# Performance work log

Measured on AMD Instinct MI355X. Metric: run time of the kernel, lower is better.

## Reference

```python
import jax, jax.numpy as jnp
import numpy as np

B, S, H = 2, 4096, 2048
NH, HD = 16, 128
BLOCK = 256
EPS = 1e-5


def setup_inputs() -> dict:
    key = jax.random.key(0)
    ks = jax.random.split(key, 6)
    return {
        "hidden_states": jax.random.normal(ks[0], (B, S, H), jnp.float32),
        "attention_mask": jnp.ones((B, S), jnp.float32),
        "slope_rate": jax.random.uniform(ks[1], (NH,), jnp.float32),
        "w_qkv": jax.random.normal(ks[2], (H, 3 * NH * HD), jnp.float32) * 0.02,
        "w_gate": jax.random.normal(ks[3], (H, NH * HD), jnp.float32) * 0.02,
        "w_out": jax.random.normal(ks[4], (NH * HD, H), jnp.float32) * 0.02,
        "norm_weight": jnp.ones((NH * HD,), jnp.float32),
    }


def _lightning_attention(q, k, v, slope):
    # q,k,v: [b,h,n,d]; slope: [h] positive decay rates
    b, h, n, d = q.shape
    nc = n // BLOCK
    ar = jnp.arange(BLOCK, dtype=q.dtype) + 1.0  # 1..BLOCK
    s = slope[:, None, None]  # [h,1,1]
    q_decay = jnp.exp(-s * ar[None, :, None])             # [h,BLOCK,1]
    k_decay = jnp.exp(-s * (BLOCK - ar)[None, :, None])   # [h,BLOCK,1]
    idx = ar[:, None] - ar[None, :]                        # [BLOCK,BLOCK]
    mask = (idx >= 0).astype(q.dtype)
    # mask idx before exp so masked entries don't overflow (keeps grads finite)
    diag_decay = jnp.exp(-s * (idx * mask)[None]) * mask[None]  # [h,BLOCK,BLOCK]
    block_decay = jnp.exp(-slope * BLOCK)[None, :, None, None]  # [1,h,1,1]

    def to_chunks(x):
        return x.reshape(b, h, nc, BLOCK, d).transpose(2, 0, 1, 3, 4)

    qc, kc, vc = to_chunks(q), to_chunks(k), to_chunks(v)

    def step(kv, xs):
        qi, ki, vi = xs  # [b,h,BLOCK,d]
        # inter-chunk: decayed query against carried state kv [b,h,d,d]
        o_inter = jnp.einsum("bhmd,bhde->bhme", qi * q_decay, kv)
        # intra-chunk: causal decayed attention
        attn = jnp.einsum("bhmd,bhnd->bhmn", qi, ki) * diag_decay
        o = o_inter + jnp.einsum("bhmn,bhne->bhme", attn, vi)
        kv = block_decay * kv + jnp.einsum("bhnd,bhne->bhde", ki * k_decay, vi)
        return kv, o

    kv0 = jnp.zeros((b, h, d, d), q.dtype)
    _, o = jax.lax.scan(step, kv0, (qc, kc, vc))  # o: [nc,b,h,BLOCK,d]
    return o.transpose(1, 2, 0, 3, 4).reshape(b, h, n, d)


def reference(hidden_states, attention_mask, slope_rate, w_qkv, w_gate, w_out, norm_weight):
    b, n, _ = hidden_states.shape
    qkv = jax.nn.silu(hidden_states @ w_qkv)  # act on fused qkv
    q, k, v = jnp.split(qkv, 3, axis=-1)

    def heads(x):
        return x.reshape(b, n, NH, HD).transpose(0, 2, 1, 3)

    q, k, v = heads(q), heads(k), heads(v)
    v = v * attention_mask[:, None, :, None]  # zero padded tokens
    o = _lightning_attention(q, k, v, slope_rate)  # [b,h,n,d]
    o = o.transpose(0, 2, 1, 3).reshape(b, n, NH * HD)
    # RMSNorm over head_dim*num_heads
    var = jnp.mean(o * o, axis=-1, keepdims=True)
    o = o * jax.lax.rsqrt(var + EPS) * norm_weight
    # sigmoid output gate from raw hidden_states
    o = jax.nn.sigmoid(hidden_states @ w_gate) * o
    return o @ w_out
```

## Files before the change

kernel.cpp:

```cpp
#include <hip/hip_runtime.h>
#include <cstdint>

#define B_ 2
#define S_ 4096
#define H_ 2048
#define NH_ 16
#define HD_ 128
#define BLOCK_ 256
#define NC_ (S_/BLOCK_)
#define M_ (B_*S_)
#define EPS_ 1e-5f

typedef unsigned short ushort_t;
typedef unsigned short u16x4 __attribute__((ext_vector_type(4)));
typedef short frag_ab __attribute__((ext_vector_type(8)));
typedef float frag_cd __attribute__((ext_vector_type(4)));

static __device__ inline float bf2f(ushort_t u) {
    union { unsigned int i; float f; } x;
    x.i = ((unsigned int)u) << 16;
    return x.f;
}
static __device__ inline ushort_t f2bf(float f) {
    union { float f; unsigned int i; } x;
    x.f = f;
    unsigned int r = x.i + 0x7fffu + ((x.i >> 16) & 1u);
    return (ushort_t)(r >> 16);
}

static __device__ __forceinline__ void gload_lds16(const ushort_t* g, ushort_t* l) {
    __builtin_amdgcn_global_load_lds(
        (__attribute__((address_space(1))) void*)(uintptr_t)g,
        (__attribute__((address_space(3))) void*)l,
        16, 0, 0);
}

#define FENCE_ asm volatile("" ::: "memory")
#define VMW0_  asm volatile("s_waitcnt vmcnt(0)" ::: "memory")

__global__ __launch_bounds__(256)
void cast_bf16_kernel(const float* __restrict__ in, ushort_t* __restrict__ out)
{
    int i = blockIdx.x * 256 + threadIdx.x;
    float4 v = reinterpret_cast<const float4*>(in)[i];
    u16x4 o = { f2bf(v.x), f2bf(v.y), f2bf(v.z), f2bf(v.w) };
    *reinterpret_cast<u16x4*>(&out[(size_t)i * 4]) = o;
}

__global__ __launch_bounds__(256)
void transpose_cast_kernel(const float* __restrict__ W, ushort_t* __restrict__ WT,
                           int K, int N)
{
    __shared__ float t[32][33];
    const int kb = blockIdx.y * 32, nb = blockIdx.x * 32;
    const int tx = threadIdx.x & 31, ty = threadIdx.x >> 5;
    #pragma unroll
    for (int i = 0; i < 4; ++i)
        t[ty + i * 8][tx] = W[(size_t)(kb + ty + i * 8) * N + nb + tx];
    __syncthreads();
    #pragma unroll
    for (int i = 0; i < 4; ++i)
        WT[(size_t)(nb + ty + i * 8) * K + kb + tx] = f2bf(t[tx][ty + i * 8]);
}

template<int MODE>
__global__ __launch_bounds__(512, 2)
void gemm256(const ushort_t* __restrict__ A, const ushort_t* __restrict__ BT,
             int M, int N, int K,
             float* __restrict__ Cf,
             ushort_t* __restrict__ qo, ushort_t* __restrict__ ko,
             ushort_t* __restrict__ kTo, ushort_t* __restrict__ vTo,
             ushort_t* __restrict__ gateo, const float* __restrict__ mask)
{
    __shared__ __align__(16) ushort_t LA[2][16384];
    __shared__ __align__(16) ushort_t LB[2][16384];

    const int tid  = threadIdx.x;
    const int lane = tid & 63, wid = tid >> 6;
    const int wm = wid >> 2, wn = wid & 3;
    const int l15 = lane & 15, l4 = lane >> 4;
    const int trow = tid >> 3;
    const int xk   = (tid & 7) ^ (trow & 7);

    const int lin = blockIdx.x;
    const int NBX = N >> 8;
    const int bxw = NBX >> 3;
    const int xcd = lin & 7, cc = lin >> 3;
    const int sh  = (bxw == 4) ? 2 : 0;
    const int by  = cc >> sh;
    const int bxi = cc & (bxw - 1);
    const int bx  = xcd * bxw + bxi;
    const int rowBase = by * 256, colBase = bx * 256;

    frag_cd acc[8][4];
    #pragma unroll
    for (int m = 0; m < 8; ++m)
        #pragma unroll
        for (int n = 0; n < 4; ++n) acc[m][n] = 0.f;

    frag_ab fa[4][2];
    frag_ab fb[2][2][2];

    #define RDF(Lp, row_, sl_) \
        (*reinterpret_cast<const frag_ab*>( \
            reinterpret_cast<const char*>(Lp) + (row_) * 128 + ((((sl_) ^ ((row_) & 7)) & 7) << 4)))
    #define STG(Gp, base_, i_, kt_, Lp) \
        gload_lds16((Gp) + (size_t)((base_) + (i_) * 64 + trow) * K + (kt_) + xk * 8, \
                    (Lp) + (i_) * 4096 + wid * 512)

    const int NT = K >> 6;
    int cur = 0;
    STG(BT, colBase, 0, 0, LB[0]); STG(BT, colBase, 1, 0, LB[0]);
    STG(BT, colBase, 2, 0, LB[0]); STG(BT, colBase, 3, 0, LB[0]);
    STG(A,  rowBase, 0, 0, LA[0]); STG(A,  rowBase, 1, 0, LA[0]);
    STG(A,  rowBase, 2, 0, LA[0]); STG(A,  rowBase, 3, 0, LA[0]);
    VMW0_; FENCE_; __builtin_amdgcn_s_barrier();
    __builtin_amdgcn_sched_barrier(0);

    for (int t = 0; t < NT; ++t) {
        const ushort_t* Ab = LA[cur];
        const ushort_t* Bb = LB[cur];
        ushort_t* An = LA[cur ^ 1];
        ushort_t* Bn = LB[cur ^ 1];
        const int ktn = (t + 1) << 6;
        const bool more = (t + 1) < NT;

        if (more) {
            STG(BT, colBase, 0, ktn, Bn); STG(BT, colBase, 1, ktn, Bn);
            STG(BT, colBase, 2, ktn, Bn); STG(BT, colBase, 3, ktn, Bn);
            STG(A,  rowBase, 0, ktn, An); STG(A,  rowBase, 1, ktn, An);
            STG(A,  rowBase, 2, ktn, An); STG(A,  rowBase, 3, ktn, An);
        }

        #pragma unroll
        for (int mi = 0; mi < 4; ++mi)
            #pragma unroll
            for (int ks = 0; ks < 2; ++ks)
                fa[mi][ks] = RDF(Ab, wm * 128 + mi * 16 + l15, ks * 4 + l4);
        #pragma unroll
        for (int ni = 0; ni < 2; ++ni)
            #pragma unroll
            for (int ks = 0; ks < 2; ++ks)
                fb[0][ni][ks] = RDF(Bb, wn * 64 + ni * 16 + l15, ks * 4 + l4);
        __builtin_amdgcn_s_setprio(1);
        #pragma unroll
        for (int mi = 0; mi < 4; ++mi)
            #pragma unroll
            for (int ni = 0; ni < 2; ++ni)
                #pragma unroll
                for (int ks = 0; ks < 2; ++ks)
                    acc[mi][ni] = __builtin_amdgcn_mfma_f32_16x16x32_bf16(
                        fa[mi][ks], fb[0][ni][ks], acc[mi][ni], 0, 0, 0);
        __builtin_amdgcn_s_setprio(0);

        #pragma unroll
        for (int ni = 0; ni < 2; ++ni)
            #pragma unroll
            for (int ks = 0; ks < 2; ++ks)
                fb[1][ni][ks] = RDF(Bb, wn * 64 + 32 + ni * 16 + l15, ks * 4 + l4);
        __builtin_amdgcn_s_setprio(1);
        #pragma unroll
        for (int mi = 0; mi < 4; ++mi)
            #pragma unroll
            for (int ni = 0; ni < 2; ++ni)
                #pragma unroll
                for (int ks = 0; ks < 2; ++ks)
                    acc[mi][2 + ni] = __builtin_amdgcn_mfma_f32_16x16x32_bf16(
                        fa[mi][ks], fb[1][ni][ks], acc[mi][2 + ni], 0, 0, 0);
        __builtin_amdgcn_s_setprio(0);

        #pragma unroll
        for (int mi = 0; mi < 4; ++mi)
            #pragma unroll
            for (int ks = 0; ks < 2; ++ks)
                fa[mi][ks] = RDF(Ab, wm * 128 + 64 + mi * 16 + l15, ks * 4 + l4);
        __builtin_amdgcn_s_setprio(1);
        #pragma unroll
        for (int mi = 0; mi < 4; ++mi)
            #pragma unroll
            for (int ni = 0; ni < 2; ++ni)
                #pragma unroll
                for (int ks = 0; ks < 2; ++ks)
                    acc[4 + mi][ni] = __builtin_amdgcn_mfma_f32_16x16x32_bf16(
                        fa[mi][ks], fb[0][ni][ks], acc[4 + mi][ni], 0, 0, 0);
        __builtin_amdgcn_s_setprio(0);

        __builtin_amdgcn_s_setprio(1);
        #pragma unroll
        for (int mi = 0; mi < 4; ++mi)
            #pragma unroll
            for (int ni = 0; ni < 2; ++ni)
                #pragma unroll
                for (int ks = 0; ks < 2; ++ks)
                    acc[4 + mi][2 + ni] = __builtin_amdgcn_mfma_f32_16x16x32_bf16(
                        fa[mi][ks], fb[1][ni][ks], acc[4 + mi][2 + ni], 0, 0, 0);
        __builtin_amdgcn_s_setprio(0);

        VMW0_; FENCE_; __builtin_amdgcn_s_barrier();
        __builtin_amdgcn_sched_barrier(0);
        cur ^= 1;
    }
    #undef RDF
    #undef STG

    const int row0 = rowBase + wm * 128;
    const int c0   = colBase + wn * 64;
    if (MODE == 0) {
        #pragma unroll
        for (int m = 0; m < 8; ++m) {
            int mr = (m >> 2) * 64 + (m & 3) * 16;
            #pragma unroll
            for (int n = 0; n < 4; ++n) {
                int nc = (n >> 1) * 32 + (n & 1) * 16;
                #pragma unroll
                for (int r = 0; r < 4; ++r) {
                    int row = row0 + mr + l4 * 4 + r;
                    int col = c0 + nc + l15;
                    Cf[(size_t)row * N + col] = acc[m][n][r];
                }
            }
        }
    } else {
        const int which = c0 >> 11;
        const int h     = (c0 >> 7) & 15;
        const int d0    = c0 & 127;
        const int b     = row0 >> 12;
        const int bh    = b * NH_ + h;
        #pragma unroll
        for (int m = 0; m < 8; ++m) {
            int mr = (m >> 2) * 64 + (m & 3) * 16;
            int sr0 = (row0 & 4095) + mr + l4 * 4;
            #pragma unroll
            for (int n = 0; n < 4; ++n) {
                int nc = (n >> 1) * 32 + (n & 1) * 16;
                float x0 = acc[m][n][0], x1 = acc[m][n][1];
                float x2 = acc[m][n][2], x3 = acc[m][n][3];
                if (which == 3) {
                    int col_g = (c0 - 6144) + nc + l15;
                    ushort_t* gp = gateo + (size_t)(row0 + mr + l4 * 4) * H_ + col_g;
                    gp[0]       = f2bf(1.f / (1.f + __expf(-x0)));
                    gp[H_]      = f2bf(1.f / (1.f + __expf(-x1)));
                    gp[2 * H_]  = f2bf(1.f / (1.f + __expf(-x2)));
                    gp[3 * H_]  = f2bf(1.f / (1.f + __expf(-x3)));
                } else {
                    int d = d0 + nc + l15;
                    float s0 = x0 / (1.f + __expf(-x0));
                    float s1 = x1 / (1.f + __expf(-x1));
                    float s2 = x2 / (1.f + __expf(-x2));
                    float s3 = x3 / (1.f + __expf(-x3));
                    if (which == 0) {
                        ushort_t* qp = qo + ((size_t)bh * S_ + sr0) * HD_ + d;
                        qp[0]        = f2bf(s0);
                        qp[HD_]      = f2bf(s1);
                        qp[2 * HD_]  = f2bf(s2);
                        qp[3 * HD_]  = f2bf(s3);
                    } else if (which == 1) {
                        u16x4 pk = { f2bf(s0), f2bf(s1), f2bf(s2), f2bf(s3) };
                        ushort_t* kp = ko + ((size_t)bh * S_ + sr0) * HD_ + d;
                        kp[0] = pk[0]; kp[HD_] = pk[1]; kp[2 * HD_] = pk[2]; kp[3 * HD_] = pk[3];
                        *reinterpret_cast<u16x4*>(&kTo[((size_t)bh * HD_ + d) * S_ + sr0]) = pk;
                    } else {
                        float mk0 = mask[b * S_ + sr0],     mk1 = mask[b * S_ + sr0 + 1];
                        float mk2 = mask[b * S_ + sr0 + 2], mk3 = mask[b * S_ + sr0 + 3];
                        u16x4 pk = { f2bf(s0 * mk0), f2bf(s1 * mk1), f2bf(s2 * mk2), f2bf(s3 * mk3) };
                        *reinterpret_cast<u16x4*>(&vTo[((size_t)bh * HD_ + d) * S_ + sr0]) = pk;
                    }
                }
            }
        }
    }
}

__global__ __launch_bounds__(256)
void kv_chunk_mfma(const ushort_t* __restrict__ kT, const ushort_t* __restrict__ vT,
                   const float* __restrict__ slope, ushort_t* __restrict__ kvT)
{
    const int c = blockIdx.x, bh = blockIdx.y;
    const float s = slope[bh & 15];
    const int tid = threadIdx.x, lane = tid & 63, w = tid >> 6;
    const int l15 = lane & 15, l4 = lane >> 4;
    __shared__ float dec[BLOCK_];
    __shared__ __align__(16) ushort_t VTl[128 * 64];
    __shared__ __align__(16) ushort_t KTl[128 * 64];
    dec[tid] = __expf(-s * (float)(BLOCK_ - 1 - tid));

    frag_cd acc[2][8];
    #pragma unroll
    for (int mf = 0; mf < 2; ++mf)
        #pragma unroll
        for (int df = 0; df < 8; ++df) acc[mf][df] = 0.f;

    for (int nt = 0; nt < 4; ++nt) {
        __syncthreads();
        #pragma unroll
        for (int i = 0; i < 4; ++i) {
            int u = tid + i * 256;
            int row = u >> 3, slot = u & 7;
            size_t gsrc = ((size_t)bh * HD_ + row) * S_ + c * BLOCK_ + nt * 64 + slot * 8;
            frag_ab v8 = *reinterpret_cast<const frag_ab*>(vT + gsrc);
            *reinterpret_cast<frag_ab*>((char*)VTl + row * 128 + ((slot * 16) ^ ((row & 7) << 4))) = v8;
            frag_ab k8 = *reinterpret_cast<const frag_ab*>(kT + gsrc);
            frag_ab kd;
            #pragma unroll
            for (int j = 0; j < 8; ++j)
                kd[j] = (short)f2bf(bf2f((ushort_t)k8[j]) * dec[nt * 64 + slot * 8 + j]);
            *reinterpret_cast<frag_ab*>((char*)KTl + row * 128 + ((slot * 16) ^ ((row & 7) << 4))) = kd;
        }
        __syncthreads();
        #pragma unroll
        for (int ks = 0; ks < 2; ++ks) {
            frag_ab a[2];
            #pragma unroll
            for (int mf = 0; mf < 2; ++mf)
                a[mf] = *reinterpret_cast<const frag_ab*>(
                    (char*)VTl + (w * 32 + mf * 16 + l15) * 128 + ((ks * 64 + l4 * 16) ^ ((l15 & 7) << 4)));
            #pragma unroll
            for (int df = 0; df < 8; ++df) {
                frag_ab bk = *reinterpret_cast<const frag_ab*>(
                    (char*)KTl + (df * 16 + l15) * 128 + ((ks * 64 + l4 * 16) ^ ((l15 & 7) << 4)));
                acc[0][df] = __builtin_amdgcn_mfma_f32_16x16x32_bf16(a[0], bk, acc[0][df], 0, 0, 0);
                acc[1][df] = __builtin_amdgcn_mfma_f32_16x16x32_bf16(a[1], bk, acc[1][df], 0, 0, 0);
            }
        }
    }
    ushort_t* out = kvT + ((size_t)bh * NC_ + c) * 16384;
    #pragma unroll
    for (int mf = 0; mf < 2; ++mf)
        #pragma unroll
        for (int df = 0; df < 8; ++df)
            #pragma unroll
            for (int r = 0; r < 4; ++r) {
                int e = w * 32 + mf * 16 + l4 * 4 + r;
                int d = df * 16 + l15;
                out[e * 128 + d] = f2bf(acc[mf][df][r]);
            }
}

__global__ __launch_bounds__(256)
void kv_scan_kernel(const float* __restrict__ slope, const ushort_t* __restrict__ kvT,
                    ushort_t* __restrict__ sT)
{
    const int es = blockIdx.x, bh = blockIdx.y;
    const float s = slope[bh & 15];
    const float bd = __expf(-s * (float)BLOCK_);
    const int tid = threadIdx.x;
    float st[16];
    #pragma unroll
    for (int i = 0; i < 16; ++i) st[i] = 0.f;
    for (int c = 0; c < NC_; ++c) {
        const ushort_t* p = kvT + ((size_t)bh * NC_ + c) * 16384;
        ushort_t* qp = sT + ((size_t)bh * NC_ + c) * 16384;
        #pragma unroll
        for (int i = 0; i < 16; ++i) {
            int lin = tid + i * 256;
            int off = (lin >> 5) * 128 + es * 32 + (lin & 31);
            float x = bf2f(p[off]);
            qp[off] = f2bf(st[i]);
            st[i] = bd * st[i] + x;
        }
    }
}

__global__ __launch_bounds__(512)
void attn_mfma(const ushort_t* __restrict__ q, const ushort_t* __restrict__ k,
               const ushort_t* __restrict__ vT, const ushort_t* __restrict__ sT,
               const float* __restrict__ slope, float* __restrict__ o)
{
    const int c = blockIdx.x, bh = blockIdx.y;
    const int h = bh & 15, b = bh >> 4;
    const float s = slope[h];
    const int tid = threadIdx.x, lane = tid & 63, w = tid >> 6;
    const int l15 = lane & 15, l4 = lane >> 4;

    __shared__ __align__(16) ushort_t SH[16384];
    __shared__ __align__(16) ushort_t P[8][2048];

    frag_ab aq[2][4];
    #pragma unroll
    for (int mf = 0; mf < 2; ++mf)
        #pragma unroll
        for (int ks = 0; ks < 4; ++ks) {
            int row = c * BLOCK_ + w * 32 + mf * 16 + l15;
            aq[mf][ks] = *reinterpret_cast<const frag_ab*>(
                q + ((size_t)bh * S_ + row) * HD_ + ks * 32 + l4 * 8);
        }

    frag_cd oa[2][8];
    #pragma unroll
    for (int mf = 0; mf < 2; ++mf)
        #pragma unroll
        for (int ef = 0; ef < 8; ++ef) oa[mf][ef] = 0.f;

    const int wrow = w * 32;
    for (int nt = 0; nt < 4; ++nt) {
        __syncthreads();
        #pragma unroll
        for (int i = 0; i < 2; ++i) {
            int u = tid + i * 512;
            int n = u >> 4, slot = u & 15;
            frag_ab k8 = *reinterpret_cast<const frag_ab*>(
                k + ((size_t)bh * S_ + c * BLOCK_ + nt * 64 + n) * HD_ + slot * 8);
            *reinterpret_cast<frag_ab*>((char*)SH + n * 256 + ((slot * 16) ^ ((n & 7) << 4))) = k8;
        }
        #pragma unroll
        for (int i = 0; i < 2; ++i) {
            int u = tid + i * 512;
            int e = u >> 3, slot = u & 7;
            frag_ab v8 = *reinterpret_cast<const frag_ab*>(
                vT + ((size_t)bh * HD_ + e) * S_ + c * BLOCK_ + nt * 64 + slot * 8);
            *reinterpret_cast<frag_ab*>((char*)SH + 16384 + e * 128 + ((slot * 16) ^ ((e & 7) << 4))) = v8;
        }
        __syncthreads();
        if (nt * 64 > wrow + 31) continue;

        frag_cd pacc[2][4];
        #pragma unroll
        for (int mf = 0; mf < 2; ++mf)
            #pragma unroll
            for (int nf = 0; nf < 4; ++nf) pacc[mf][nf] = 0.f;
        #pragma unroll
        for (int ks = 0; ks < 4; ++ks)
            #pragma unroll
            for (int nf = 0; nf < 4; ++nf) {
                frag_ab bk = *reinterpret_cast<const frag_ab*>(
                    (char*)SH + (nf * 16 + l15) * 256 + ((ks * 64 + l4 * 16) ^ ((l15 & 7) << 4)));
                pacc[0][nf] = __builtin_amdgcn_mfma_f32_16x16x32_bf16(aq[0][ks], bk, pacc[0][nf], 0, 0, 0);
                pacc[1][nf] = __builtin_amdgcn_mfma_f32_16x16x32_bf16(aq[1][ks], bk, pacc[1][nf], 0, 0, 0);
            }
        #pragma unroll
        for (int mf = 0; mf < 2; ++mf)
            #pragma unroll
            for (int nf = 0; nf < 4; ++nf)
                #pragma unroll
                for (int r = 0; r < 4; ++r) {
                    int m = mf * 16 + l4 * 4 + r;
                    int mrow = wrow + m;
                    int ncol = nt * 64 + nf * 16 + l15;
                    float pv = 0.f;
                    if (mrow >= ncol) pv = pacc[mf][nf][r] * __expf(s * (float)(ncol - mrow));
                    *reinterpret_cast<ushort_t*>(
                        (char*)&P[w][0] + m * 128 + (((nf * 16 + l15) * 2) ^ ((m & 7) << 4))) = f2bf(pv);
                }
        __builtin_amdgcn_sched_barrier(0);
        #pragma unroll
        for (int ks = 0; ks < 2; ++ks) {
            frag_ab ap[2];
            #pragma unroll
            for (int mf = 0; mf < 2; ++mf)
                ap[mf] = *reinterpret_cast<const frag_ab*>(
                    (char*)&P[w][0] + (mf * 16 + l15) * 128 + ((ks * 64 + l4 * 16) ^ ((l15 & 7) << 4)));
            #pragma unroll
            for (int ef = 0; ef < 8; ++ef) {
                frag_ab bv = *reinterpret_cast<const frag_ab*>(
                    (char*)SH + 16384 + (ef * 16 + l15) * 128 + ((ks * 64 + l4 * 16) ^ ((l15 & 7) << 4)));
                oa[0][ef] = __builtin_amdgcn_mfma_f32_16x16x32_bf16(ap[0], bv, oa[0][ef], 0, 0, 0);
                oa[1][ef] = __builtin_amdgcn_mfma_f32_16x16x32_bf16(ap[1], bv, oa[1][ef], 0, 0, 0);
            }
        }
    }

    __syncthreads();
    #pragma unroll
    for (int i = 0; i < 4; ++i) {
        int u = tid + i * 512;
        int e = u >> 4, slot = u & 15;
        frag_ab s8 = *reinterpret_cast<const frag_ab*>(
            sT + ((size_t)(bh * NC_ + c)) * 16384 + e * 128 + slot * 8);
        *reinterpret_cast<frag_ab*>((char*)SH + e * 256 + ((slot * 16) ^ ((e & 7) << 4))) = s8;
    }
    __syncthreads();
    #pragma unroll
    for (int mf = 0; mf < 2; ++mf) {
        float qd = __expf(-s * (float)(wrow + mf * 16 + l15 + 1));
        #pragma unroll
        for (int ks = 0; ks < 4; ++ks) {
            frag_ab v = aq[mf][ks];
            #pragma unroll
            for (int j = 0; j < 8; ++j)
                v[j] = (short)f2bf(bf2f((ushort_t)v[j]) * qd);
            aq[mf][ks] = v;
        }
    }
    #pragma unroll
    for (int ks = 0; ks < 4; ++ks)
        #pragma unroll
        for (int ef = 0; ef < 8; ++ef) {
            frag_ab bs = *reinterpret_cast<const frag_ab*>(
                (char*)SH + (ef * 16 + l15) * 256 + ((ks * 64 + l4 * 16) ^ ((l15 & 7) << 4)));
            oa[0][ef] = __builtin_amdgcn_mfma_f32_16x16x32_bf16(aq[0][ks], bs, oa[0][ef], 0, 0, 0);
            oa[1][ef] = __builtin_amdgcn_mfma_f32_16x16x32_bf16(aq[1][ks], bs, oa[1][ef], 0, 0, 0);
        }
    #pragma unroll
    for (int mf = 0; mf < 2; ++mf)
        #pragma unroll
        for (int ef = 0; ef < 8; ++ef)
            #pragma unroll
            for (int r = 0; r < 4; ++r) {
                int row = c * BLOCK_ + wrow + mf * 16 + l4 * 4 + r;
                int col = h * HD_ + ef * 16 + l15;
                o[((size_t)(b * S_ + row)) * H_ + col] = oa[mf][ef][r];
            }
}

__global__ __launch_bounds__(256)
void norm_gate_kernel(const float* __restrict__ o, const ushort_t* __restrict__ gate,
                      const float* __restrict__ nw, ushort_t* __restrict__ on)
{
    const int row = blockIdx.x;
    const int tid = threadIdx.x;
    const float* orow = o + (size_t)row * H_;
    const ushort_t* grow = gate + (size_t)row * H_;
    ushort_t* onrow = on + (size_t)row * H_;
    float vals[8];
    float ss = 0.f;
    #pragma unroll
    for (int i = 0; i < 8; ++i) {
        vals[i] = orow[tid + i * 256];
        ss += vals[i] * vals[i];
    }
    __shared__ float red[256];
    red[tid] = ss;
    __syncthreads();
    #pragma unroll
    for (int st = 128; st > 0; st >>= 1) {
        if (tid < st) red[tid] += red[tid + st];
        __syncthreads();
    }
    float scale = rsqrtf(red[0] * (1.f / (float)H_) + EPS_);
    #pragma unroll
    for (int i = 0; i < 8; ++i) {
        int cidx = tid + i * 256;
        onrow[cidx] = f2bf(vals[i] * scale * nw[cidx] * bf2f(grow[cidx]));
    }
}

extern "C" void kernel_launch(void* const* d_in, const int* in_sizes, int n_in,
                              void* d_out, int out_size, void* d_ws, size_t ws_size,
                              hipStream_t stream)
{
    const float* hidden = (const float*)d_in[0];
    const float* mask   = (const float*)d_in[1];
    const float* slope  = (const float*)d_in[2];
    const float* w_qkv  = (const float*)d_in[3];
    const float* w_gate = (const float*)d_in[4];
    const float* w_out  = (const float*)d_in[5];
    const float* nw     = (const float*)d_in[6];

    const size_t MH = (size_t)M_ * H_;
    ushort_t* hid_bf  = (ushort_t*)d_ws;
    ushort_t* on_ws   = hid_bf;
    ushort_t* wqkvT   = hid_bf + MH;
    ushort_t* wgateT  = wqkvT + (size_t)6144 * 2048;
    ushort_t* kvT_ws  = wqkvT;
    ushort_t* sT_ws   = wqkvT + MH / 2;
    ushort_t* woutT   = wqkvT;
    ushort_t* q_ws    = hid_bf + 2 * MH;
    ushort_t* k_ws    = q_ws + MH;
    ushort_t* vT_ws   = k_ws + MH;
    ushort_t* gate_ws = vT_ws + MH;
    ushort_t* kT_ws   = (ushort_t*)d_out;
    float*    o_f32   = (float*)d_out;

    dim3 blk(256);
    cast_bf16_kernel<<<(MH / 4) / 256, blk, 0, stream>>>(hidden, hid_bf);
    transpose_cast_kernel<<<dim3(6144 / 32, 2048 / 32), blk, 0, stream>>>(w_qkv, wqkvT, 2048, 6144);
    transpose_cast_kernel<<<dim3(2048 / 32, 2048 / 32), blk, 0, stream>>>(w_gate, wgateT, 2048, 2048);
    gemm256<2><<<dim3((M_ / 256) * (8192 / 256)), dim3(512), 0, stream>>>(
        hid_bf, wqkvT, M_, 8192, 2048,
        nullptr, q_ws, k_ws, kT_ws, vT_ws, gate_ws, mask);
    kv_chunk_mfma<<<dim3(NC_, B_ * NH_), blk, 0, stream>>>(kT_ws, vT_ws, slope, kvT_ws);
    kv_scan_kernel<<<dim3(4, B_ * NH_), blk, 0, stream>>>(slope, kvT_ws, sT_ws);
    attn_mfma<<<dim3(NC_, B_ * NH_), dim3(512), 0, stream>>>(
        q_ws, k_ws, vT_ws, sT_ws, slope, o_f32);
    transpose_cast_kernel<<<dim3(2048 / 32, 2048 / 32), blk, 0, stream>>>(w_out, woutT, 2048, 2048);
    norm_gate_kernel<<<M_, blk, 0, stream>>>(o_f32, gate_ws, nw, on_ws);
    gemm256<0><<<dim3((M_ / 256) * (2048 / 256)), dim3(512), 0, stream>>>(
        on_ws, woutT, M_, 2048, 2048,
        (float*)d_out, nullptr, nullptr, nullptr, nullptr, nullptr, nullptr);
}
```

Measured before the change: 561.3 us.

## Switch GEMM to 4-stage K=32 LDS pipeline with partial vmcnt waits

Replaces the double-buffered K=64 tile loop in the 256x256 GEMM with a four-buffer ring of K=32 tiles, prefetching three tiles ahead. Each iteration waits only on the oldest outstanding global-to-LDS loads via vmcnt(8)/vmcnt(4) instead of draining all loads. The aim is to hide global load latency behind MFMA work. In exchange it runs twice as many iterations and barriers, does less MFMA work per barrier, and uses a narrower 4-way LDS swizzle that may raise bank conflicts.

```diff
diff --git a/kernel.cpp b/kernel.cpp
--- a/kernel.cpp
+++ b/kernel.cpp
@@ -36,6 +36,8 @@
 }
 
 #define FENCE_ asm volatile("" ::: "memory")
+#define VMW8_  asm volatile("s_waitcnt vmcnt(8)" ::: "memory")
+#define VMW4_  asm volatile("s_waitcnt vmcnt(4)" ::: "memory")
 #define VMW0_  asm volatile("s_waitcnt vmcnt(0)" ::: "memory")
 
 __global__ __launch_bounds__(256)
@@ -72,15 +74,15 @@
              ushort_t* __restrict__ kTo, ushort_t* __restrict__ vTo,
              ushort_t* __restrict__ gateo, const float* __restrict__ mask)
 {
-    __shared__ __align__(16) ushort_t LA[2][16384];
-    __shared__ __align__(16) ushort_t LB[2][16384];
+    __shared__ __align__(16) ushort_t LA[4][8192];
+    __shared__ __align__(16) ushort_t LB[4][8192];
 
     const int tid  = threadIdx.x;
     const int lane = tid & 63, wid = tid >> 6;
     const int wm = wid >> 2, wn = wid & 3;
     const int l15 = lane & 15, l4 = lane >> 4;
-    const int trow = tid >> 3;
-    const int xk   = (tid & 7) ^ (trow & 7);
+    const int trow = tid >> 2;
+    const int xk   = (tid & 3) ^ (trow & 3);
 
     const int lin = blockIdx.x;
     const int NBX = N >> 8;
@@ -98,107 +100,69 @@
         #pragma unroll
         for (int n = 0; n < 4; ++n) acc[m][n] = 0.f;
 
-    frag_ab fa[4][2];
-    frag_ab fb[2][2][2];
+    frag_ab fa[4];
+    frag_ab fb[4];
 
     #define RDF(Lp, row_, sl_) \
         (*reinterpret_cast<const frag_ab*>( \
-            reinterpret_cast<const char*>(Lp) + (row_) * 128 + ((((sl_) ^ ((row_) & 7)) & 7) << 4)))
+            reinterpret_cast<const char*>(Lp) + (row_) * 64 + ((((sl_) ^ ((row_) & 3)) & 3) << 4)))
     #define STG(Gp, base_, i_, kt_, Lp) \
-        gload_lds16((Gp) + (size_t)((base_) + (i_) * 64 + trow) * K + (kt_) + xk * 8, \
+        gload_lds16((Gp) + (size_t)((base_) + (i_) * 128 + trow) * K + (kt_) + xk * 8, \
                     (Lp) + (i_) * 4096 + wid * 512)
 
-    const int NT = K >> 6;
-    int cur = 0;
-    STG(BT, colBase, 0, 0, LB[0]); STG(BT, colBase, 1, 0, LB[0]);
-    STG(BT, colBase, 2, 0, LB[0]); STG(BT, colBase, 3, 0, LB[0]);
-    STG(A,  rowBase, 0, 0, LA[0]); STG(A,  rowBase, 1, 0, LA[0]);
-    STG(A,  rowBase, 2, 0, LA[0]); STG(A,  rowBase, 3, 0, LA[0]);
-    VMW0_; FENCE_; __builtin_amdgcn_s_barrier();
+    const int NT = K >> 5;
+    #pragma unroll
+    for (int j = 0; j < 3; ++j) {
+        STG(BT, colBase, 0, j * 32, LB[j]); STG(BT, colBase, 1, j * 32, LB[j]);
+        STG(A,  rowBase, 0, j * 32, LA[j]); STG(A,  rowBase, 1, j * 32, LA[j]);
+    }
+    VMW8_;
+    FENCE_; __builtin_amdgcn_s_barrier();
     __builtin_amdgcn_sched_barrier(0);
 
     for (int t = 0; t < NT; ++t) {
-        const ushort_t* Ab = LA[cur];
-        const ushort_t* Bb = LB[cur];
-        ushort_t* An = LA[cur ^ 1];
-        ushort_t* Bn = LB[cur ^ 1];
-        const int ktn = (t + 1) << 6;
-        const bool more = (t + 1) < NT;
-
-        if (more) {
-            STG(BT, colBase, 0, ktn, Bn); STG(BT, colBase, 1, ktn, Bn);
-            STG(BT, colBase, 2, ktn, Bn); STG(BT, colBase, 3, ktn, Bn);
-            STG(A,  rowBase, 0, ktn, An); STG(A,  rowBase, 1, ktn, An);
-            STG(A,  rowBase, 2, ktn, An); STG(A,  rowBase, 3, ktn, An);
-        }
-
+        const int ri = t & 3, si = (t + 3) & 3;
+        const ushort_t* Ab = &LA[ri][0];
+        const ushort_t* Bb = &LB[ri][0];
+        const int ktn = (t + 3) << 5;
+
+        if (t + 3 < NT) {
+            STG(BT, colBase, 0, ktn, &LB[si][0]); STG(BT, colBase, 1, ktn, &LB[si][0]);
+            STG(A,  rowBase, 0, ktn, &LA[si][0]); STG(A,  rowBase, 1, ktn, &LA[si][0]);
+        }
+
+        #pragma unroll
+        for (int nf = 0; nf < 4; ++nf)
+            fb[nf] = RDF(Bb, wn * 64 + nf * 16 + l15, l4);
         #pragma unroll
         for (int mi = 0; mi < 4; ++mi)
-            #pragma unroll
-            for (int ks = 0; ks < 2; ++ks)
-                fa[mi][ks] = RDF(Ab, wm * 128 + mi * 16 + l15, ks * 4 + l4);
-        #pragma unroll
-        for (int ni = 0; ni < 2; ++ni)
-            #pragma unroll
-            for (int ks = 0; ks < 2; ++ks)
-                fb[0][ni][ks] = RDF(Bb, wn * 64 + ni * 16 + l15, ks * 4 + l4);
+            fa[mi] = RDF(Ab, wm * 128 + mi * 16 + l15, l4);
         __builtin_amdgcn_s_setprio(1);
         #pragma unroll
         for (int mi = 0; mi < 4; ++mi)
             #pragma unroll
-            for (int ni = 0; ni < 2; ++ni)
-                #pragma unroll
-                for (int ks = 0; ks < 2; ++ks)
-                    acc[mi][ni] = __builtin_amdgcn_mfma_f32_16x16x32_bf16(
-                        fa[mi][ks], fb[0][ni][ks], acc[mi][ni], 0, 0, 0);
+            for (int nf = 0; nf < 4; ++nf)
+                acc[mi][nf] = __builtin_amdgcn_mfma_f32_16x16x32_bf16(
+                    fa[mi], fb[nf], acc[mi][nf], 0, 0, 0);
         __builtin_amdgcn_s_setprio(0);
 
         #pragma unroll
-        for (int ni = 0; ni < 2; ++ni)
-            #pragma unroll
-            for (int ks = 0; ks < 2; ++ks)
-                fb[1][ni][ks] = RDF(Bb, wn * 64 + 32 + ni * 16 + l15, ks * 4 + l4);
+        for (int mi = 0; mi < 4; ++mi)
+            fa[mi] = RDF(Ab, wm * 128 + 64 + mi * 16 + l15, l4);
         __builtin_amdgcn_s_setprio(1);
         #pragma unroll
         for (int mi = 0; mi < 4; ++mi)
             #pragma unroll
-            for (int ni = 0; ni < 2; ++ni)
-                #pragma unroll
-                for (int ks = 0; ks < 2; ++ks)
-                    acc[mi][2 + ni] = __builtin_amdgcn_mfma_f32_16x16x32_bf16(
-                        fa[mi][ks], fb[1][ni][ks], acc[mi][2 + ni], 0, 0, 0);
+            for (int nf = 0; nf < 4; ++nf)
+                acc[4 + mi][nf] = __builtin_amdgcn_mfma_f32_16x16x32_bf16(
+                    fa[mi], fb[nf], acc[4 + mi][nf], 0, 0, 0);
         __builtin_amdgcn_s_setprio(0);
 
-        #pragma unroll
-        for (int mi = 0; mi < 4; ++mi)
-            #pragma unroll
-            for (int ks = 0; ks < 2; ++ks)
-                fa[mi][ks] = RDF(Ab, wm * 128 + 64 + mi * 16 + l15, ks * 4 + l4);
-        __builtin_amdgcn_s_setprio(1);
-        #pragma unroll
-        for (int mi = 0; mi < 4; ++mi)
-            #pragma unroll
-            for (int ni = 0; ni < 2; ++ni)
-                #pragma unroll
-                for (int ks = 0; ks < 2; ++ks)
-                    acc[4 + mi][ni] = __builtin_amdgcn_mfma_f32_16x16x32_bf16(
-                        fa[mi][ks], fb[0][ni][ks], acc[4 + mi][ni], 0, 0, 0);
-        __builtin_amdgcn_s_setprio(0);
-
-        __builtin_amdgcn_s_setprio(1);
-        #pragma unroll
-        for (int mi = 0; mi < 4; ++mi)
-            #pragma unroll
-            for (int ni = 0; ni < 2; ++ni)
-                #pragma unroll
-                for (int ks = 0; ks < 2; ++ks)
-                    acc[4 + mi][2 + ni] = __builtin_amdgcn_mfma_f32_16x16x32_bf16(
-                        fa[mi][ks], fb[1][ni][ks], acc[4 + mi][2 + ni], 0, 0, 0);
-        __builtin_amdgcn_s_setprio(0);
-
-        VMW0_; FENCE_; __builtin_amdgcn_s_barrier();
+        if (t + 3 < NT)      { VMW8_; }
+        else if (t + 2 < NT) { VMW4_; }
+        else                 { VMW0_; }
+        FENCE_; __builtin_amdgcn_s_barrier();
         __builtin_amdgcn_sched_barrier(0);
-        cur ^= 1;
     }
     #undef RDF
     #undef STG
@@ -211,7 +175,7 @@
             int mr = (m >> 2) * 64 + (m & 3) * 16;
             #pragma unroll
             for (int n = 0; n < 4; ++n) {
-                int nc = (n >> 1) * 32 + (n & 1) * 16;
+                int nc = n * 16;
                 #pragma unroll
                 for (int r = 0; r < 4; ++r) {
                     int row = row0 + mr + l4 * 4 + r;
@@ -232,7 +196,7 @@
             int sr0 = (row0 & 4095) + mr + l4 * 4;
             #pragma unroll
             for (int n = 0; n < 4; ++n) {
-                int nc = (n >> 1) * 32 + (n & 1) * 16;
+                int nc = n * 16;
                 float x0 = acc[m][n][0], x1 = acc[m][n][1];
                 float x2 = acc[m][n][2], x3 = acc[m][n][3];
                 if (which == 3) {
```

New measurement: 639.3 us. 13.9% more time.

## Shrink GEMM tiles to 128x128 with 256-thread blocks and XCD-aware remap

Applied to the files above, without the earlier changes.

Replaces the 256x256-tile, 512-thread GEMM with a 128x128-tile, 256-thread version (4 waves, each computing 64x64), halving LDS use. The block index is remapped so consecutive tiles land on the same XCD. The aim is more workgroups and better occupancy and load balance across CUs. The cost is lower arithmetic intensity per tile and more global and LDS traffic per FLOP.

```diff
diff --git a/kernel.cpp b/kernel.cpp
--- a/kernel.cpp
+++ b/kernel.cpp
@@ -64,56 +64,51 @@
 }
 
 template<int MODE>
-__global__ __launch_bounds__(512, 2)
-void gemm256(const ushort_t* __restrict__ A, const ushort_t* __restrict__ BT,
+__global__ __launch_bounds__(256, 2)
+void gemm128(const ushort_t* __restrict__ A, const ushort_t* __restrict__ BT,
              int M, int N, int K,
              float* __restrict__ Cf,
              ushort_t* __restrict__ qo, ushort_t* __restrict__ ko,
              ushort_t* __restrict__ kTo, ushort_t* __restrict__ vTo,
              ushort_t* __restrict__ gateo, const float* __restrict__ mask)
 {
-    __shared__ __align__(16) ushort_t LA[2][16384];
-    __shared__ __align__(16) ushort_t LB[2][16384];
+    __shared__ __align__(16) ushort_t LA[2][8192];
+    __shared__ __align__(16) ushort_t LB[2][8192];
 
     const int tid  = threadIdx.x;
     const int lane = tid & 63, wid = tid >> 6;
-    const int wm = wid >> 2, wn = wid & 3;
+    const int wm = wid >> 1, wn = wid & 1;
     const int l15 = lane & 15, l4 = lane >> 4;
     const int trow = tid >> 3;
     const int xk   = (tid & 7) ^ (trow & 7);
 
+    const int nwg = gridDim.x;
     const int lin = blockIdx.x;
-    const int NBX = N >> 8;
-    const int bxw = NBX >> 3;
-    const int xcd = lin & 7, cc = lin >> 3;
-    const int sh  = (bxw == 4) ? 2 : 0;
-    const int by  = cc >> sh;
-    const int bxi = cc & (bxw - 1);
-    const int bx  = xcd * bxw + bxi;
-    const int rowBase = by * 256, colBase = bx * 256;
-
-    frag_cd acc[8][4];
-    #pragma unroll
-    for (int m = 0; m < 8; ++m)
+    const int virt = (lin & 7) * (nwg >> 3) + (lin >> 3);
+    const int NBX = N >> 7;
+    const int by = virt / NBX, bx = virt - by * NBX;
+    const int rowBase = by * 128, colBase = bx * 128;
+
+    frag_cd acc[4][4];
+    #pragma unroll
+    for (int m = 0; m < 4; ++m)
         #pragma unroll
         for (int n = 0; n < 4; ++n) acc[m][n] = 0.f;
 
     frag_ab fa[4][2];
-    frag_ab fb[2][2][2];
+    frag_ab fb[4][2];
 
     #define RDF(Lp, row_, sl_) \
         (*reinterpret_cast<const frag_ab*>( \
             reinterpret_cast<const char*>(Lp) + (row_) * 128 + ((((sl_) ^ ((row_) & 7)) & 7) << 4)))
     #define STG(Gp, base_, i_, kt_, Lp) \
-        gload_lds16((Gp) + (size_t)((base_) + (i_) * 64 + trow) * K + (kt_) + xk * 8, \
-                    (Lp) + (i_) * 4096 + wid * 512)
+        gload_lds16((Gp) + (size_t)((base_) + (i_) * 32 + trow) * K + (kt_) + xk * 8, \
+                    (Lp) + (i_) * 2048 + wid * 512)
 
     const int NT = K >> 6;
     int cur = 0;
-    STG(BT, colBase, 0, 0, LB[0]); STG(BT, colBase, 1, 0, LB[0]);
-    STG(BT, colBase, 2, 0, LB[0]); STG(BT, colBase, 3, 0, LB[0]);
-    STG(A,  rowBase, 0, 0, LA[0]); STG(A,  rowBase, 1, 0, LA[0]);
-    STG(A,  rowBase, 2, 0, LA[0]); STG(A,  rowBase, 3, 0, LA[0]);
+    #pragma unroll
+    for (int i = 0; i < 4; ++i) { STG(A, rowBase, i, 0, LA[0]); STG(BT, colBase, i, 0, LB[0]); }
     VMW0_; FENCE_; __builtin_amdgcn_s_barrier();
     __builtin_amdgcn_sched_barrier(0);
 
@@ -126,74 +121,30 @@
         const bool more = (t + 1) < NT;
 
         if (more) {
-            STG(BT, colBase, 0, ktn, Bn); STG(BT, colBase, 1, ktn, Bn);
-            STG(BT, colBase, 2, ktn, Bn); STG(BT, colBase, 3, ktn, Bn);
-            STG(A,  rowBase, 0, ktn, An); STG(A,  rowBase, 1, ktn, An);
-            STG(A,  rowBase, 2, ktn, An); STG(A,  rowBase, 3, ktn, An);
-        }
-
+            #pragma unroll
+            for (int i = 0; i < 4; ++i) { STG(A, rowBase, i, ktn, An); STG(BT, colBase, i, ktn, Bn); }
+        }
+
+        #pragma unroll
+        for (int ni = 0; ni < 4; ++ni)
+            #pragma unroll
+            for (int ks = 0; ks < 2; ++ks)
+                fb[ni][ks] = RDF(Bb, wn * 64 + ni * 16 + l15, ks * 4 + l4);
         #pragma unroll
         for (int mi = 0; mi < 4; ++mi)
             #pragma unroll
             for (int ks = 0; ks < 2; ++ks)
-                fa[mi][ks] = RDF(Ab, wm * 128 + mi * 16 + l15, ks * 4 + l4);
-        #pragma unroll
-        for (int ni = 0; ni < 2; ++ni)
-            #pragma unroll
-            for (int ks = 0; ks < 2; ++ks)
-                fb[0][ni][ks] = RDF(Bb, wn * 64 + ni * 16 + l15, ks * 4 + l4);
+                fa[mi][ks] = RDF(Ab, wm * 64 + mi * 16 + l15, ks * 4 + l4);
+
         __builtin_amdgcn_s_setprio(1);
         #pragma unroll
         for (int mi = 0; mi < 4; ++mi)
             #pragma unroll
-            for (int ni = 0; ni < 2; ++ni)
+            for (int ni = 0; ni < 4; ++ni)
                 #pragma unroll
                 for (int ks = 0; ks < 2; ++ks)
                     acc[mi][ni] = __builtin_amdgcn_mfma_f32_16x16x32_bf16(
-                        fa[mi][ks], fb[0][ni][ks], acc[mi][ni], 0, 0, 0);
-        __builtin_amdgcn_s_setprio(0);
-
-        #pragma unroll
-        for (int ni = 0; ni < 2; ++ni)
-            #pragma unroll
-            for (int ks = 0; ks < 2; ++ks)
-                fb[1][ni][ks] = RDF(Bb, wn * 64 + 32 + ni * 16 + l15, ks * 4 + l4);
-        __builtin_amdgcn_s_setprio(1);
-        #pragma unroll
-        for (int mi = 0; mi < 4; ++mi)
-            #pragma unroll
-            for (int ni = 0; ni < 2; ++ni)
-                #pragma unroll
-                for (int ks = 0; ks < 2; ++ks)
-                    acc[mi][2 + ni] = __builtin_amdgcn_mfma_f32_16x16x32_bf16(
-                        fa[mi][ks], fb[1][ni][ks], acc[mi][2 + ni], 0, 0, 0);
-        __builtin_amdgcn_s_setprio(0);
-
-        #pragma unroll
-        for (int mi = 0; mi < 4; ++mi)
-            #pragma unroll
-            for (int ks = 0; ks < 2; ++ks)
-                fa[mi][ks] = RDF(Ab, wm * 128 + 64 + mi * 16 + l15, ks * 4 + l4);
-        __builtin_amdgcn_s_setprio(1);
-        #pragma unroll
-        for (int mi = 0; mi < 4; ++mi)
-            #pragma unroll
-            for (int ni = 0; ni < 2; ++ni)
-                #pragma unroll
-                for (int ks = 0; ks < 2; ++ks)
-                    acc[4 + mi][ni] = __builtin_amdgcn_mfma_f32_16x16x32_bf16(
-                        fa[mi][ks], fb[0][ni][ks], acc[4 + mi][ni], 0, 0, 0);
-        __builtin_amdgcn_s_setprio(0);
-
-        __builtin_amdgcn_s_setprio(1);
-        #pragma unroll
-        for (int mi = 0; mi < 4; ++mi)
-            #pragma unroll
-            for (int ni = 0; ni < 2; ++ni)
-                #pragma unroll
-                for (int ks = 0; ks < 2; ++ks)
-                    acc[4 + mi][2 + ni] = __builtin_amdgcn_mfma_f32_16x16x32_bf16(
-                        fa[mi][ks], fb[1][ni][ks], acc[4 + mi][2 + ni], 0, 0, 0);
+                        fa[mi][ks], fb[ni][ks], acc[mi][ni], 0, 0, 0);
         __builtin_amdgcn_s_setprio(0);
 
         VMW0_; FENCE_; __builtin_amdgcn_s_barrier();
@@ -203,19 +154,17 @@
     #undef RDF
     #undef STG
 
-    const int row0 = rowBase + wm * 128;
+    const int row0 = rowBase + wm * 64;
     const int c0   = colBase + wn * 64;
     if (MODE == 0) {
         #pragma unroll
-        for (int m = 0; m < 8; ++m) {
-            int mr = (m >> 2) * 64 + (m & 3) * 16;
+        for (int m = 0; m < 4; ++m) {
             #pragma unroll
             for (int n = 0; n < 4; ++n) {
-                int nc = (n >> 1) * 32 + (n & 1) * 16;
                 #pragma unroll
                 for (int r = 0; r < 4; ++r) {
-                    int row = row0 + mr + l4 * 4 + r;
-                    int col = c0 + nc + l15;
+                    int row = row0 + m * 16 + l4 * 4 + r;
+                    int col = c0 + n * 16 + l15;
                     Cf[(size_t)row * N + col] = acc[m][n][r];
                 }
             }
@@ -227,23 +176,21 @@
         const int b     = row0 >> 12;
         const int bh    = b * NH_ + h;
         #pragma unroll
-        for (int m = 0; m < 8; ++m) {
-            int mr = (m >> 2) * 64 + (m & 3) * 16;
-            int sr0 = (row0 & 4095) + mr + l4 * 4;
+        for (int m = 0; m < 4; ++m) {
+            int sr0 = (row0 & 4095) + m * 16 + l4 * 4;
             #pragma unroll
             for (int n = 0; n < 4; ++n) {
-                int nc = (n >> 1) * 32 + (n & 1) * 16;
                 float x0 = acc[m][n][0], x1 = acc[m][n][1];
                 float x2 = acc[m][n][2], x3 = acc[m][n][3];
                 if (which == 3) {
-                    int col_g = (c0 - 6144) + nc + l15;
-                    ushort_t* gp = gateo + (size_t)(row0 + mr + l4 * 4) * H_ + col_g;
+                    int col_g = (c0 - 6144) + n * 16 + l15;
+                    ushort_t* gp = gateo + (size_t)(row0 + m * 16 + l4 * 4) * H_ + col_g;
                     gp[0]       = f2bf(1.f / (1.f + __expf(-x0)));
                     gp[H_]      = f2bf(1.f / (1.f + __expf(-x1)));
                     gp[2 * H_]  = f2bf(1.f / (1.f + __expf(-x2)));
                     gp[3 * H_]  = f2bf(1.f / (1.f + __expf(-x3)));
                 } else {
-                    int d = d0 + nc + l15;
+                    int d = d0 + n * 16 + l15;
                     float s0 = x0 / (1.f + __expf(-x0));
                     float s1 = x1 / (1.f + __expf(-x1));
                     float s2 = x2 / (1.f + __expf(-x2));
@@ -565,7 +512,7 @@
     cast_bf16_kernel<<<(MH / 4) / 256, blk, 0, stream>>>(hidden, hid_bf);
     transpose_cast_kernel<<<dim3(6144 / 32, 2048 / 32), blk, 0, stream>>>(w_qkv, wqkvT, 2048, 6144);
     transpose_cast_kernel<<<dim3(2048 / 32, 2048 / 32), blk, 0, stream>>>(w_gate, wgateT, 2048, 2048);
-    gemm256<2><<<dim3((M_ / 256) * (8192 / 256)), dim3(512), 0, stream>>>(
+    gemm128<2><<<dim3((M_ / 128) * (8192 / 128)), blk, 0, stream>>>(
         hid_bf, wqkvT, M_, 8192, 2048,
         nullptr, q_ws, k_ws, kT_ws, vT_ws, gate_ws, mask);
     kv_chunk_mfma<<<dim3(NC_, B_ * NH_), blk, 0, stream>>>(kT_ws, vT_ws, slope, kvT_ws);
@@ -574,7 +521,7 @@
         q_ws, k_ws, vT_ws, sT_ws, slope, o_f32);
     transpose_cast_kernel<<<dim3(2048 / 32, 2048 / 32), blk, 0, stream>>>(w_out, woutT, 2048, 2048);
     norm_gate_kernel<<<M_, blk, 0, stream>>>(o_f32, gate_ws, nw, on_ws);
-    gemm256<0><<<dim3((M_ / 256) * (2048 / 256)), dim3(512), 0, stream>>>(
+    gemm128<0><<<dim3((M_ / 128) * (2048 / 128)), blk, 0, stream>>>(
         on_ws, woutT, M_, 2048, 2048,
         (float*)d_out, nullptr, nullptr, nullptr, nullptr, nullptr, nullptr);
 }
```

Measured after the change: 591.8 us. 1.05x slower.
